# Kernel tuning notes

Hardware: AMD Instinct MI355X
Metric: run time of the kernel (lower is better)

## Reference

```python
import jax, jax.numpy as jnp
import numpy as np

E = 192      # embed_dim
DI = 384     # d_inner = 2*E (mamba default expand=2)
S = 16       # d_state
R = 12       # dt_rank = ceil(E/16)
DEPTH = 4
STRIDE = 4
P = 400      # num_patches = 1600/4
NC = 20
BATCH = 32
EPS = 1e-5


def _rmsnorm(x, w):
    x = x.astype(jnp.float32)
    return x * jax.lax.rsqrt(jnp.mean(x * x, axis=-1, keepdims=True) + EPS) * w


def _mamba_mixer(h, in_w, cw, cb, xpw, dtw, dtb, a_log, d_skip, ow):
    # h: [B, L, E]
    Bsz, Ln, _ = h.shape
    xz = jnp.einsum('ble,de->bld', h, in_w)            # [B,L,2*DI]
    xm, z = xz[..., :DI], xz[..., DI:]
    # causal depthwise conv1d, kernel 4 (left pad 3, truncate to L)
    xp = jnp.pad(xm, ((0, 0), (3, 0), (0, 0)))
    xc = sum(xp[:, k:k + Ln, :] * cw[:, k] for k in range(4)) + cb
    xc = jax.nn.silu(xc)
    xdb = jnp.einsum('bld,rd->blr', xc, xpw)           # [B,L,R+2S]
    dt = jax.nn.softplus(jnp.einsum('blr,dr->bld', xdb[..., :R], dtw) + dtb)
    Bm = xdb[..., R:R + S]
    Cm = xdb[..., R + S:]
    A = -jnp.exp(a_log)                                # [DI,S]

    def step(hst, inp):
        dt_t, b_t, c_t, u_t = inp                      # [B,DI],[B,S],[B,S],[B,DI]
        dA = jnp.exp(dt_t[:, :, None] * A)             # [B,DI,S]
        hst = dA * hst + (dt_t * u_t)[:, :, None] * b_t[:, None, :]
        y_t = jnp.einsum('bdn,bn->bd', hst, c_t)
        return hst, y_t

    h0 = jnp.zeros((Bsz, DI, S), xc.dtype)
    xs = (dt.transpose(1, 0, 2), Bm.transpose(1, 0, 2), Cm.transpose(1, 0, 2), xc.transpose(1, 0, 2))
    _, ys = jax.lax.scan(step, h0, xs)
    y = ys.transpose(1, 0, 2) + xc * d_skip
    y = y * jax.nn.silu(z)
    return jnp.einsum('bld,ed->ble', y, ow)


def _forward(imgs, patch_w, patch_b, cls_token, pos_embed, cnn_w, cnn_b, norm_w,
             in_proj_w, conv_w, conv_b, x_proj_w, dt_proj_w, dt_proj_b, A_log, D,
             out_proj_w, norm_f_w, head_w, head_b):
    Bsz = imgs.shape[0]
    # StrideEmbed: conv1d kernel=stride=4 == reshape + matmul
    x = imgs.reshape(Bsz, P, STRIDE)
    x = jnp.einsum('blk,ek->ble', x, patch_w[:, 0, :]) + patch_b   # [B,P,E]
    x = x + pos_embed[:, :-1, :]
    # depthwise conv1d k=3 pad=1 over length
    xp = jnp.pad(x, ((0, 0), (1, 1), (0, 0)))
    x = sum(xp[:, k:k + P, :] * cnn_w[:, 0, k] for k in range(3)) + cnn_b
    cls = cls_token + pos_embed[:, -1, :]                           # [1,1,E]
    x = jnp.concatenate([x, jnp.broadcast_to(cls, (Bsz, 1, E))], axis=1)  # [B,401,E]

    hidden = x
    residual = None
    for i in range(DEPTH):
        residual = hidden if residual is None else residual + hidden
        hn = _rmsnorm(residual, norm_w[i])
        hidden = _mamba_mixer(hn, in_proj_w[i], conv_w[i], conv_b[i], x_proj_w[i],
                              dt_proj_w[i], dt_proj_b[i], A_log[i], D[i], out_proj_w[i])
    out = _rmsnorm(hidden + residual, norm_f_w)
    v_sem = out[:, -1, :]
    return v_sem @ head_w.T + head_b


def setup_inputs() -> dict:
    key = jax.random.key(0)
    ks = jax.random.split(key, 12)
    n = lambda k, shp, s=0.02: jax.random.normal(k, shp, dtype=jnp.float32) * s
    return {
        'imgs': jax.random.normal(ks[0], (BATCH, 1, 40, 40), jnp.float32),
        'patch_w': n(ks[1], (E, 1, STRIDE), 0.3),
        'patch_b': jnp.zeros((E,), jnp.float32),
        'cls_token': n(ks[2], (1, 1, E)),
        'pos_embed': n(ks[3], (1, P + 1, E)),
        'cnn_w': n(ks[4], (E, 1, 3), 0.3),
        'cnn_b': jnp.zeros((E,), jnp.float32),
        'norm_w': jnp.ones((DEPTH, E), jnp.float32),
        'in_proj_w': n(ks[5], (DEPTH, 2 * DI, E), 0.05),
        'conv_w': n(ks[6], (DEPTH, DI, 4), 0.3),
        'conv_b': jnp.zeros((DEPTH, DI), jnp.float32),
        'x_proj_w': n(ks[7], (DEPTH, R + 2 * S, DI), 0.05),
        'dt_proj_w': n(ks[8], (DEPTH, DI, R), 0.3),
        'dt_proj_b': jnp.log(jnp.expm1(jax.random.uniform(ks[9], (DEPTH, DI), minval=0.001, maxval=0.1))),
        'A_log': jnp.log(jnp.broadcast_to(jnp.arange(1, S + 1, dtype=jnp.float32), (DEPTH, DI, S))),
        'D': jnp.ones((DEPTH, DI), jnp.float32),
        'out_proj_w': n(ks[10], (DEPTH, E, DI), 0.05),
        'norm_f_w': jnp.ones((E,), jnp.float32),
        'head_w': n(ks[11], (NC, E)),
        'head_b': jnp.zeros((NC,), jnp.float32),
    }


def reference(imgs, patch_w, patch_b, cls_token, pos_embed, cnn_w, cnn_b, norm_w,
              in_proj_w, conv_w, conv_b, x_proj_w, dt_proj_w, dt_proj_b, A_log, D,
              out_proj_w, norm_f_w, head_w, head_b):
    return _forward(imgs, patch_w, patch_b, cls_token, pos_embed, cnn_w, cnn_b, norm_w,
                    in_proj_w, conv_w, conv_b, x_proj_w, dt_proj_w, dt_proj_b, A_log, D,
                    out_proj_w, norm_f_w, head_w, head_b)
```

## Files before the change

kernel.cpp:

```cpp
#include <hip/hip_runtime.h>
#include <math.h>

#define E 192
#define DI 384
#define S 16
#define R 12
#define DEPTH 4
#define P 400
#define NC 20
#define BATCH 32
#define L 401
#define NTOK (BATCH * L)
#define CH 32
#define NCH 13

using short8 = __attribute__((ext_vector_type(8))) short;
using float4v = __attribute__((ext_vector_type(4))) float;

__device__ __forceinline__ float siluf(float x) {
    return x / (1.f + __expf(-x));
}
__device__ __forceinline__ float softplusf(float x) {
    return (x > 20.f) ? x : log1pf(__expf(x));
}
__device__ __forceinline__ unsigned short f2bf(float x) {
    unsigned int u = __float_as_uint(x);
    unsigned int r = 0x7fffu + ((u >> 16) & 1u);
    return (unsigned short)((u + r) >> 16);
}
__device__ __forceinline__ float bf2f(unsigned short v) {
    return __uint_as_float(((unsigned int)v) << 16);
}

__global__ void k_embed(const float* __restrict__ imgs, const float* __restrict__ patch_w,
                        const float* __restrict__ patch_b, const float* __restrict__ cls_token,
                        const float* __restrict__ pos_embed, const float* __restrict__ cnn_w,
                        const float* __restrict__ cnn_b, float* __restrict__ resid) {
    int idx = blockIdx.x * blockDim.x + threadIdx.x;
    if (idx >= NTOK * E) return;
    int e = idx % E;
    int bl = idx / E;
    int l = bl % L;
    int b = bl / L;
    float out;
    if (l == P) {
        out = cls_token[e] + pos_embed[(size_t)P * E + e];
    } else {
        float w0 = patch_w[e * 4 + 0], w1 = patch_w[e * 4 + 1];
        float w2 = patch_w[e * 4 + 2], w3 = patch_w[e * 4 + 3];
        float pb = patch_b[e];
        const float* ib = imgs + (size_t)b * 1600;
        auto xe = [&](int ll) -> float {
            const float* ip = ib + ll * 4;
            return ip[0] * w0 + ip[1] * w1 + ip[2] * w2 + ip[3] * w3 + pb +
                   pos_embed[(size_t)ll * E + e];
        };
        float c0 = cnn_w[e * 3 + 0], c1 = cnn_w[e * 3 + 1], c2 = cnn_w[e * 3 + 2];
        float acc = cnn_b[e] + xe(l) * c1;
        if (l > 0) acc += xe(l - 1) * c0;
        if (l < P - 1) acc += xe(l + 1) * c2;
        out = acc;
    }
    resid[idx] = out;
}

__global__ void k_rmsnorm(const float* __restrict__ resid, unsigned short* __restrict__ hn,
                          const float* __restrict__ w) {
    int wave = blockIdx.x * (blockDim.x >> 6) + (threadIdx.x >> 6);
    int lane = threadIdx.x & 63;
    if (wave >= NTOK) return;
    size_t base = (size_t)wave * E;
    float v[3];
    float ss = 0.f;
#pragma unroll
    for (int j = 0; j < 3; j++) {
        int e = lane + j * 64;
        float r = resid[base + e];
        v[j] = r;
        ss += r * r;
    }
#pragma unroll
    for (int off = 32; off > 0; off >>= 1) ss += __shfl_xor(ss, off, 64);
    float scale = rsqrtf(ss * (1.f / (float)E) + 1e-5f);
#pragma unroll
    for (int j = 0; j < 3; j++) {
        int e = lane + j * 64;
        hn[base + e] = f2bf(v[j] * scale * w[e]);
    }
}

__global__ void k_prep(const float* __restrict__ in_proj_w, const float* __restrict__ x_proj_w,
                       const float* __restrict__ out_proj_w, const float* __restrict__ A_log,
                       const float* __restrict__ dt_proj_w,
                       unsigned short* __restrict__ w_in, unsigned short* __restrict__ w_x,
                       unsigned short* __restrict__ w_out, float* __restrict__ negA,
                       float* __restrict__ dtw_t) {
    const int n1 = DEPTH * 2 * DI * E;
    const int n2 = DEPTH * 44 * DI;
    const int n3 = DEPTH * E * DI;
    const int n4 = DEPTH * DI * S;
    const int n5 = DEPTH * DI * R;
    int idx = blockIdx.x * blockDim.x + threadIdx.x;
    if (idx < n1) {
        w_in[idx] = f2bf(in_proj_w[idx]);
    } else if (idx < n1 + n2) {
        int i = idx - n1;
        w_x[i] = f2bf(x_proj_w[i]);
    } else if (idx < n1 + n2 + n3) {
        int i = idx - n1 - n2;
        w_out[i] = f2bf(out_proj_w[i]);
    } else if (idx < n1 + n2 + n3 + n4) {
        int i = idx - n1 - n2 - n3;
        int layer = i / (DI * S);
        int rem = i % (DI * S);
        int n = rem / DI;
        int d = rem % DI;
        negA[i] = -__expf(A_log[(size_t)layer * DI * S + d * S + n]);
    } else if (idx < n1 + n2 + n3 + n4 + n5) {
        int i = idx - n1 - n2 - n3 - n4;
        int layer = i / (DI * R);
        int rem = i % (DI * R);
        int r = rem / DI;
        int d = rem % DI;
        dtw_t[i] = dt_proj_w[(size_t)layer * DI * R + d * R + r];
    }
}

__global__ void k_flag(const float* __restrict__ negA, int* __restrict__ flag) {
    int idx = blockIdx.x * blockDim.x + threadIdx.x;
    if (idx >= DEPTH * DI) return;
    int layer = idx / DI;
    int d = idx % DI;
    const float* base = negA + (size_t)layer * DI * S;
    float a0 = base[d];
    bool ok = true;
#pragma unroll
    for (int n = 1; n < S; n++) {
        float an = base[n * DI + d];
        ok = ok && (fabsf(an - (float)(n + 1) * a0) <= 1e-5f * fabsf(an));
    }
    flag[idx] = ok ? 1 : 0;
}

template <int BM, int BN, int BK, int EPI>
__global__ __launch_bounds__(256) void k_gemm_bf16(const unsigned short* __restrict__ A,
                                                   const unsigned short* __restrict__ W,
                                                   float* __restrict__ C,
                                                   unsigned short* __restrict__ XM,
                                                   unsigned short* __restrict__ Z,
                                                   int M, int N, int K) {
    constexpr int PADK = BK + 8;
    constexpr int MT = BM / 32, NT = BN / 32;
    __shared__ unsigned short As[BM][PADK];
    __shared__ unsigned short Bs[BN][PADK];
    int tid = threadIdx.x;
    int m0 = blockIdx.y * BM, n0 = blockIdx.x * BN;
    int wave = tid >> 6, lane = tid & 63;
    int row16 = lane & 15, quad = lane >> 4;
    int wm0 = (wave >> 1) * (BM / 2), wn0 = (wave & 1) * (BN / 2);

    float4v acc[MT][NT];
#pragma unroll
    for (int i = 0; i < MT; i++)
#pragma unroll
        for (int j = 0; j < NT; j++) acc[i][j] = (float4v){0.f, 0.f, 0.f, 0.f};

    for (int k0 = 0; k0 < K; k0 += BK) {
#pragma unroll
        for (int idx = tid * 8; idx < BM * BK; idx += 256 * 8) {
            int row = idx / BK, col = idx % BK;
            int gm = m0 + row;
            short8 v;
            if (gm < M)
                v = *(const short8*)&A[(size_t)gm * K + k0 + col];
            else
                v = (short8)0;
            *(short8*)&As[row][col] = v;
        }
#pragma unroll
        for (int idx = tid * 8; idx < BN * BK; idx += 256 * 8) {
            int row = idx / BK, col = idx % BK;
            int gn = n0 + row;
            short8 v;
            if (gn < N)
                v = *(const short8*)&W[(size_t)gn * K + k0 + col];
            else
                v = (short8)0;
            *(short8*)&Bs[row][col] = v;
        }
        __syncthreads();
#pragma unroll
        for (int kk = 0; kk < BK; kk += 32) {
            int koff = kk + quad * 8;
            short8 af[MT], bfr[NT];
#pragma unroll
            for (int i = 0; i < MT; i++)
                af[i] = *(const short8*)&As[wm0 + i * 16 + row16][koff];
#pragma unroll
            for (int j = 0; j < NT; j++)
                bfr[j] = *(const short8*)&Bs[wn0 + j * 16 + row16][koff];
#pragma unroll
            for (int i = 0; i < MT; i++)
#pragma unroll
                for (int j = 0; j < NT; j++)
                    acc[i][j] = __builtin_amdgcn_mfma_f32_16x16x32_bf16(af[i], bfr[j],
                                                                        acc[i][j], 0, 0, 0);
        }
        __syncthreads();
    }
#pragma unroll
    for (int i = 0; i < MT; i++) {
#pragma unroll
        for (int j = 0; j < NT; j++) {
#pragma unroll
            for (int r = 0; r < 4; r++) {
                int m = m0 + wm0 + i * 16 + quad * 4 + r;
                int n = n0 + wn0 + j * 16 + row16;
                if (m >= M || n >= N) continue;
                float v = acc[i][j][r];
                if (EPI == 0) {
                    C[(size_t)m * N + n] = v;
                } else if (EPI == 1) {
                    if (n < DI)
                        XM[(size_t)m * DI + n] = f2bf(v);
                    else
                        Z[(size_t)m * DI + (n - DI)] = f2bf(v);
                } else {
                    C[(size_t)m * N + n] += v;
                }
            }
        }
    }
}

__global__ void k_conv(const unsigned short* __restrict__ xm_bf, const float* __restrict__ cw,
                       const float* __restrict__ cb, unsigned short* __restrict__ xc_bf) {
    int idx = blockIdx.x * blockDim.x + threadIdx.x;
    if (idx >= NTOK * DI) return;
    int d = idx % DI;
    int bl = idx / DI;
    int l = bl % L;
    int b = bl / L;
    const unsigned short* base = xm_bf + (size_t)b * L * DI + d;
    float acc = cb[d];
#pragma unroll
    for (int k = 0; k < 4; k++) {
        int ll = l - 3 + k;
        if (ll >= 0) acc += bf2f(base[(size_t)ll * DI]) * cw[d * 4 + k];
    }
    xc_bf[idx] = f2bf(siluf(acc));
}

__global__ __launch_bounds__(384) void k_dtpre(
        const float* __restrict__ xdb, const float* __restrict__ dtw_t,
        const float* __restrict__ dtb, float* __restrict__ dtbuf) {
    int tok = blockIdx.x;
    int d = threadIdx.x;
    const float* xr = xdb + (size_t)tok * 44;
    float acc = dtb[d];
#pragma unroll
    for (int r = 0; r < R; r++) acc += xr[r] * dtw_t[r * DI + d];
    dtbuf[(size_t)tok * DI + d] = softplusf(acc);
}

template <bool LAST>
__global__ __launch_bounds__(384) void k_scanA(
        const unsigned short* __restrict__ xc_bf, const float* __restrict__ xdb,
        const float* __restrict__ dtbuf, const float* __restrict__ negA_l,
        const int* __restrict__ flag_l, const float* __restrict__ Dskip,
        float2* __restrict__ ydt, float* __restrict__ hend) {
    int d = threadIdx.x;
    int ch = blockIdx.x;
    int b = blockIdx.y;
    int t0 = ch * CH;
    int t1 = min(t0 + CH, L);
    bool fast = __all(flag_l[d] != 0);
    float a0 = negA_l[d];
    float a[S];
    if (!fast) {
#pragma unroll
        for (int n = 0; n < S; n++) a[n] = negA_l[n * DI + d];
    }
    float dsk = Dskip[d];
    float h[S] = {};
    float dts = 0.f;
    size_t tok0 = (size_t)b * L + t0;
    float dt_nx = dtbuf[tok0 * DI + d];
    float u_nx = bf2f(xc_bf[tok0 * DI + d]);
    float e1_nx = __expf(a0 * dt_nx);
    for (int t = t0; t < t1; t++) {
        size_t tok = (size_t)b * L + t;
        float dtv = dt_nx, e1v = e1_nx, uu = u_nx;
        if (t + 1 < t1) {
            dt_nx = dtbuf[(tok + 1) * DI + d];
            u_nx = bf2f(xc_bf[(tok + 1) * DI + d]);
            e1_nx = __expf(a0 * dt_nx);
        }
        const float* row = xdb + tok * 44;
        dts += dtv;
        float dtu = dtv * uu;
        float y = uu * dsk;
        if (fast) {
            float p = e1v;
#pragma unroll
            for (int n = 0; n < S; n++) {
                h[n] = p * h[n] + dtu * row[R + n];
                y += h[n] * row[R + S + n];
                p *= e1v;
            }
        } else {
#pragma unroll
            for (int n = 0; n < S; n++) {
                float dA = __expf(dtv * a[n]);
                h[n] = dA * h[n] + dtu * row[R + n];
                y += h[n] * row[R + S + n];
            }
        }
        if (!LAST || t == P || t == t1 - 1) ydt[tok * DI + d] = make_float2(y, dts);
    }
    float* he = hend + ((size_t)(b * NCH + ch) * S) * DI + d;
#pragma unroll
    for (int n = 0; n < S; n++) he[n * DI] = h[n];
}

__global__ __launch_bounds__(384) void k_fixup(
        const unsigned short* __restrict__ z_bf, const float* __restrict__ xdb,
        const float* __restrict__ negA_l, const int* __restrict__ flag_l,
        const float* __restrict__ hend, const float2* __restrict__ ydt,
        unsigned short* __restrict__ y_bf) {
    int d = threadIdx.x;
    int ch = blockIdx.x;
    int b = blockIdx.y;
    bool fast = __all(flag_l[d] != 0);
    float a0 = negA_l[d];
    float a[S];
    if (!fast) {
#pragma unroll
        for (int n = 0; n < S; n++) a[n] = negA_l[n * DI + d];
    }
    float h0[S] = {};
    for (int c = 0; c < ch; c++) {
        size_t o = ((size_t)(b * NCH + c) * S) * DI + d;
        int tlast = min(c * CH + CH, L) - 1;
        float dts = ydt[((size_t)b * L + tlast) * DI + d].y;
        if (fast) {
            float e1c = __expf(a0 * dts);
            float p = e1c;
#pragma unroll
            for (int n = 0; n < S; n++) {
                h0[n] = p * h0[n] + hend[o + n * DI];
                p *= e1c;
            }
        } else {
#pragma unroll
            for (int n = 0; n < S; n++) h0[n] = __expf(dts * a[n]) * h0[n] + hend[o + n * DI];
        }
    }
    int t0 = ch * CH, t1 = min(t0 + CH, L);
    for (int t = t0; t < t1; t++) {
        size_t idx = ((size_t)b * L + t) * DI + d;
        float2 yd = ydt[idx];
        float y = yd.x;
        if (ch != 0) {
            const float* cv = xdb + ((size_t)b * L + t) * 44 + R + S;
            float dts = yd.y;
            float corr = 0.f;
            if (fast) {
                float e1c = __expf(negA_l[d] * dts);
                float p = e1c;
#pragma unroll
                for (int n = 0; n < S; n++) {
                    corr += cv[n] * p * h0[n];
                    p *= e1c;
                }
            } else {
#pragma unroll
                for (int n = 0; n < S; n++)
                    corr += cv[n] * __expf(negA_l[n * DI + d] * dts) * h0[n];
            }
            y += corr;
        }
        float z = bf2f(z_bf[idx]);
        y_bf[idx] = f2bf(y * siluf(z));
    }
}

__global__ __launch_bounds__(384) void k_fixup_last(
        const unsigned short* __restrict__ z_bf, const float* __restrict__ xdb,
        const float* __restrict__ negA_l, const int* __restrict__ flag_l,
        const float* __restrict__ hend, const float2* __restrict__ ydt,
        unsigned short* __restrict__ y32) {
    int b = blockIdx.x;
    int d = threadIdx.x;
    int tok = b * L + P;
    const int ch = P / CH;
    bool fast = __all(flag_l[d] != 0);
    float a0 = negA_l[d];
    float a[S];
    if (!fast) {
#pragma unroll
        for (int n = 0; n < S; n++) a[n] = negA_l[n * DI + d];
    }
    float h0[S] = {};
    for (int c = 0; c < ch; c++) {
        size_t o = ((size_t)(b * NCH + c) * S) * DI + d;
        int tlast = min(c * CH + CH, L) - 1;
        float dts = ydt[((size_t)b * L + tlast) * DI + d].y;
        if (fast) {
            float e1c = __expf(a0 * dts);
            float p = e1c;
#pragma unroll
            for (int n = 0; n < S; n++) {
                h0[n] = p * h0[n] + hend[o + n * DI];
                p *= e1c;
            }
        } else {
#pragma unroll
            for (int n = 0; n < S; n++) h0[n] = __expf(dts * a[n]) * h0[n] + hend[o + n * DI];
        }
    }
    size_t idx = (size_t)tok * DI + d;
    float2 yd = ydt[idx];
    float y = yd.x;
    {
        const float* cv = xdb + (size_t)tok * 44 + R + S;
        float dts = yd.y;
        float corr = 0.f;
        if (fast) {
            float e1c = __expf(negA_l[d] * dts);
            float p = e1c;
#pragma unroll
            for (int n = 0; n < S; n++) {
                corr += cv[n] * p * h0[n];
                p *= e1c;
            }
        } else {
#pragma unroll
            for (int n = 0; n < S; n++)
                corr += cv[n] * __expf(negA_l[n * DI + d] * dts) * h0[n];
        }
        y += corr;
    }
    float z = bf2f(z_bf[idx]);
    y32[(size_t)b * DI + d] = f2bf(y * siluf(z));
}

__global__ void k_head(const float* __restrict__ resid, const float* __restrict__ hidden32,
                       const float* __restrict__ norm_f_w, const float* __restrict__ head_w,
                       const float* __restrict__ head_b, float* __restrict__ out) {
    __shared__ float v[E];
    int b = blockIdx.x;
    int lane = threadIdx.x;
    size_t base = ((size_t)b * L + P) * E;
    float loc[3];
    float ss = 0.f;
#pragma unroll
    for (int j = 0; j < 3; j++) {
        int e = lane + j * 64;
        float x = resid[base + e] + hidden32[(size_t)b * E + e];
        loc[j] = x;
        ss += x * x;
    }
#pragma unroll
    for (int off = 32; off > 0; off >>= 1) ss += __shfl_xor(ss, off, 64);
    float scale = rsqrtf(ss * (1.f / (float)E) + 1e-5f);
#pragma unroll
    for (int j = 0; j < 3; j++) {
        int e = lane + j * 64;
        v[e] = loc[j] * scale * norm_f_w[e];
    }
    __syncthreads();
    if (lane < NC) {
        float acc = head_b[lane];
        for (int e = 0; e < E; e++) acc += v[e] * head_w[lane * E + e];
        out[b * NC + lane] = acc;
    }
}

extern "C" void kernel_launch(void* const* d_in, const int* in_sizes, int n_in,
                              void* d_out, int out_size, void* d_ws, size_t ws_size,
                              hipStream_t stream) {
    const float* imgs      = (const float*)d_in[0];
    const float* patch_w   = (const float*)d_in[1];
    const float* patch_b   = (const float*)d_in[2];
    const float* cls_token = (const float*)d_in[3];
    const float* pos_embed = (const float*)d_in[4];
    const float* cnn_w     = (const float*)d_in[5];
    const float* cnn_b     = (const float*)d_in[6];
    const float* norm_w    = (const float*)d_in[7];
    const float* in_proj_w = (const float*)d_in[8];
    const float* conv_w    = (const float*)d_in[9];
    const float* conv_b    = (const float*)d_in[10];
    const float* x_proj_w  = (const float*)d_in[11];
    const float* dt_proj_w = (const float*)d_in[12];
    const float* dt_proj_b = (const float*)d_in[13];
    const float* A_log     = (const float*)d_in[14];
    const float* Dskip     = (const float*)d_in[15];
    const float* out_proj_w= (const float*)d_in[16];
    const float* norm_f_w  = (const float*)d_in[17];
    const float* head_w    = (const float*)d_in[18];
    const float* head_b    = (const float*)d_in[19];

    float* ws = (float*)d_ws;
    size_t off = 0;
    float* resid  = ws + off; off += (size_t)NTOK * E;
    float* xdb    = ws + off; off += (size_t)NTOK * 44;
    float* dtbuf  = ws + off; off += (size_t)NTOK * DI;
    float* ydt    = ws + off; off += (size_t)NTOK * DI * 2;
    float* hend   = ws + off; off += (size_t)BATCH * NCH * DI * S;
    float* negA   = ws + off; off += (size_t)DEPTH * DI * S;
    float* dtw_t  = ws + off; off += (size_t)DEPTH * DI * R;
    float* hid32  = ws + off; off += (size_t)BATCH * E;
    int*   gflag  = (int*)(ws + off); off += (size_t)DEPTH * DI;
    unsigned short* xm_bf  = (unsigned short*)(ws + off); off += (size_t)NTOK * DI / 2;
    unsigned short* z_bf   = (unsigned short*)(ws + off); off += (size_t)NTOK * DI / 2;
    unsigned short* bf_buf = (unsigned short*)(ws + off); off += (size_t)NTOK * DI / 2;
    unsigned short* y32_bf = (unsigned short*)(ws + off); off += (size_t)BATCH * DI / 2 + 16;
    unsigned short* w_in  = (unsigned short*)(ws + off); off += (size_t)DEPTH * 2 * DI * E / 2;
    unsigned short* w_x   = (unsigned short*)(ws + off); off += (size_t)DEPTH * 44 * DI / 2 + 16;
    unsigned short* w_out = (unsigned short*)(ws + off); off += (size_t)DEPTH * E * DI / 2;

    unsigned short* hn_bf = bf_buf;
    unsigned short* xc_bf = bf_buf;
    unsigned short* y_bf  = bf_buf;

    {
        int ntot = DEPTH * (2 * DI * E + 44 * DI + E * DI + DI * S + DI * R);
        k_prep<<<(ntot + 255) / 256, 256, 0, stream>>>(in_proj_w, x_proj_w, out_proj_w, A_log,
                                                       dt_proj_w, w_in, w_x, w_out, negA,
                                                       dtw_t);
        k_flag<<<(DEPTH * DI + 255) / 256, 256, 0, stream>>>(negA, gflag);
    }

    k_embed<<<(NTOK * E) / 256, 256, 0, stream>>>(imgs, patch_w, patch_b, cls_token,
                                                  pos_embed, cnn_w, cnn_b, resid);

    for (int i = 0; i < DEPTH; i++) {
        k_rmsnorm<<<NTOK / 4, 256, 0, stream>>>(resid, hn_bf, norm_w + i * E);

        {
            dim3 g((2 * DI) / 64, (NTOK + 127) / 128);
            k_gemm_bf16<128, 64, 64, 1><<<g, 256, 0, stream>>>(
                hn_bf, w_in + (size_t)i * 2 * DI * E, nullptr, xm_bf, z_bf, NTOK, 2 * DI, E);
        }
        k_conv<<<(NTOK * DI) / 256, 256, 0, stream>>>(xm_bf, conv_w + (size_t)i * DI * 4,
                                                      conv_b + (size_t)i * DI, xc_bf);
        {
            dim3 g(1, NTOK / 32);
            k_gemm_bf16<32, 64, 128, 0><<<g, 256, 0, stream>>>(
                xc_bf, w_x + (size_t)i * 44 * DI, xdb, nullptr, nullptr, NTOK, 44, DI);
        }
        const float* nA = negA + (size_t)i * DI * S;
        const int* fl = gflag + (size_t)i * DI;
        k_dtpre<<<NTOK, 384, 0, stream>>>(xdb, dtw_t + (size_t)i * DI * R,
                                          dt_proj_b + (size_t)i * DI, dtbuf);
        dim3 g(NCH, BATCH);
        if (i < DEPTH - 1) {
            k_scanA<false><<<g, DI, 0, stream>>>(xc_bf, xdb, dtbuf, nA, fl,
                                                 Dskip + (size_t)i * DI, (float2*)ydt, hend);
            k_fixup<<<g, DI, 0, stream>>>(z_bf, xdb, nA, fl, hend,
                                          (const float2*)ydt, y_bf);
            dim3 go(E / 64, (NTOK + 63) / 64);
            k_gemm_bf16<64, 64, 128, 2><<<go, 256, 0, stream>>>(
                y_bf, w_out + (size_t)i * E * DI, resid, nullptr, nullptr, NTOK, E, DI);
        } else {
            k_scanA<true><<<g, DI, 0, stream>>>(xc_bf, xdb, dtbuf, nA, fl,
                                                Dskip + (size_t)i * DI, (float2*)ydt, hend);
            k_fixup_last<<<BATCH, DI, 0, stream>>>(z_bf, xdb, nA, fl, hend,
                                                   (const float2*)ydt, y32_bf);
            dim3 go(E / 64, 1);
            k_gemm_bf16<32, 64, 128, 0><<<go, 256, 0, stream>>>(
                y32_bf, w_out + (size_t)i * E * DI, hid32, nullptr, nullptr, BATCH, E, DI);
        }
    }

    k_head<<<BATCH, 64, 0, stream>>>(resid, hid32, norm_f_w, head_w, head_b, (float*)d_out);
}
```

Baseline: 746.8 us.

## Fuse chunked scan and fixup into one cooperative kernel with grid sync

Merges the chunked selective-scan and the cross-chunk fixup into a single cooperative kernel. Per-chunk outputs stay in shared memory across two grid-wide syncs instead of going through the global ydt buffer. The prefix combine of chunk end states now runs once per batch in chunk-0 blocks and writes per-chunk initial states, so each chunk no longer redoes the serial combine over all earlier chunks. The change cuts one launch and a large float2 write/read round trip. In exchange it needs 416 co-resident blocks, each holding 48KB of shared memory, and adds grid-sync latency plus a serial 13-step combine phase.

```diff
diff --git a/kernel.cpp b/kernel.cpp
--- a/kernel.cpp
+++ b/kernel.cpp
@@ -1,5 +1,8 @@
 #include <hip/hip_runtime.h>
+#include <hip/hip_cooperative_groups.h>
 #include <math.h>
+
+namespace cg = cooperative_groups;
 
 #define E 192
 #define DI 384
@@ -264,11 +267,14 @@
 }
 
 template <bool LAST>
-__global__ __launch_bounds__(384) void k_scanA(
+__global__ __launch_bounds__(384, 3) void k_scan_fused(
         const unsigned short* __restrict__ xc_bf, const float* __restrict__ xdb,
         const float* __restrict__ dtbuf, const float* __restrict__ negA_l,
         const int* __restrict__ flag_l, const float* __restrict__ Dskip,
-        float2* __restrict__ ydt, float* __restrict__ hend) {
+        const unsigned short* __restrict__ z_bf,
+        float* __restrict__ hend, float* __restrict__ dtlast,
+        float* __restrict__ hinit, unsigned short* __restrict__ y_out) {
+    __shared__ float ysm[CH][DI];
     int d = threadIdx.x;
     int ch = blockIdx.x;
     int b = blockIdx.y;
@@ -282,167 +288,138 @@
         for (int n = 0; n < S; n++) a[n] = negA_l[n * DI + d];
     }
     float dsk = Dskip[d];
-    float h[S] = {};
-    float dts = 0.f;
-    size_t tok0 = (size_t)b * L + t0;
-    float dt_nx = dtbuf[tok0 * DI + d];
-    float u_nx = bf2f(xc_bf[tok0 * DI + d]);
-    float e1_nx = __expf(a0 * dt_nx);
-    for (int t = t0; t < t1; t++) {
-        size_t tok = (size_t)b * L + t;
-        float dtv = dt_nx, e1v = e1_nx, uu = u_nx;
-        if (t + 1 < t1) {
-            dt_nx = dtbuf[(tok + 1) * DI + d];
-            u_nx = bf2f(xc_bf[(tok + 1) * DI + d]);
-            e1_nx = __expf(a0 * dt_nx);
-        }
-        const float* row = xdb + tok * 44;
-        dts += dtv;
-        float dtu = dtv * uu;
-        float y = uu * dsk;
-        if (fast) {
-            float p = e1v;
-#pragma unroll
-            for (int n = 0; n < S; n++) {
-                h[n] = p * h[n] + dtu * row[R + n];
-                y += h[n] * row[R + S + n];
-                p *= e1v;
+
+    {
+        float h[S] = {};
+        float dts = 0.f;
+        size_t tok0 = (size_t)b * L + t0;
+        float dt_nx = dtbuf[tok0 * DI + d];
+        float u_nx = bf2f(xc_bf[tok0 * DI + d]);
+        float e1_nx = __expf(a0 * dt_nx);
+        for (int t = t0; t < t1; t++) {
+            size_t tok = (size_t)b * L + t;
+            float dtv = dt_nx, e1v = e1_nx, uu = u_nx;
+            if (t + 1 < t1) {
+                dt_nx = dtbuf[(tok + 1) * DI + d];
+                u_nx = bf2f(xc_bf[(tok + 1) * DI + d]);
+                e1_nx = __expf(a0 * dt_nx);
             }
-        } else {
-#pragma unroll
-            for (int n = 0; n < S; n++) {
-                float dA = __expf(dtv * a[n]);
-                h[n] = dA * h[n] + dtu * row[R + n];
-                y += h[n] * row[R + S + n];
+            const float* row = xdb + tok * 44;
+            dts += dtv;
+            float dtu = dtv * uu;
+            float y = uu * dsk;
+            if (fast) {
+                float p = e1v;
+#pragma unroll
+                for (int n = 0; n < S; n++) {
+                    h[n] = p * h[n] + dtu * row[R + n];
+                    y += h[n] * row[R + S + n];
+                    p *= e1v;
+                }
+            } else {
+#pragma unroll
+                for (int n = 0; n < S; n++) {
+                    float dA = __expf(dtv * a[n]);
+                    h[n] = dA * h[n] + dtu * row[R + n];
+                    y += h[n] * row[R + S + n];
+                }
             }
-        }
-        if (!LAST || t == P || t == t1 - 1) ydt[tok * DI + d] = make_float2(y, dts);
-    }
-    float* he = hend + ((size_t)(b * NCH + ch) * S) * DI + d;
-#pragma unroll
-    for (int n = 0; n < S; n++) he[n * DI] = h[n];
-}
-
-__global__ __launch_bounds__(384) void k_fixup(
-        const unsigned short* __restrict__ z_bf, const float* __restrict__ xdb,
-        const float* __restrict__ negA_l, const int* __restrict__ flag_l,
-        const float* __restrict__ hend, const float2* __restrict__ ydt,
-        unsigned short* __restrict__ y_bf) {
-    int d = threadIdx.x;
-    int ch = blockIdx.x;
-    int b = blockIdx.y;
-    bool fast = __all(flag_l[d] != 0);
-    float a0 = negA_l[d];
-    float a[S];
-    if (!fast) {
-#pragma unroll
-        for (int n = 0; n < S; n++) a[n] = negA_l[n * DI + d];
-    }
-    float h0[S] = {};
-    for (int c = 0; c < ch; c++) {
-        size_t o = ((size_t)(b * NCH + c) * S) * DI + d;
-        int tlast = min(c * CH + CH, L) - 1;
-        float dts = ydt[((size_t)b * L + tlast) * DI + d].y;
-        if (fast) {
-            float e1c = __expf(a0 * dts);
-            float p = e1c;
-#pragma unroll
-            for (int n = 0; n < S; n++) {
-                h0[n] = p * h0[n] + hend[o + n * DI];
-                p *= e1c;
-            }
-        } else {
-#pragma unroll
-            for (int n = 0; n < S; n++) h0[n] = __expf(dts * a[n]) * h0[n] + hend[o + n * DI];
-        }
-    }
-    int t0 = ch * CH, t1 = min(t0 + CH, L);
-    for (int t = t0; t < t1; t++) {
-        size_t idx = ((size_t)b * L + t) * DI + d;
-        float2 yd = ydt[idx];
-        float y = yd.x;
-        if (ch != 0) {
-            const float* cv = xdb + ((size_t)b * L + t) * 44 + R + S;
-            float dts = yd.y;
-            float corr = 0.f;
+            ysm[t - t0][d] = y;
+        }
+        float* he = hend + ((size_t)(b * NCH + ch) * S) * DI + d;
+#pragma unroll
+        for (int n = 0; n < S; n++) he[n * DI] = h[n];
+        dtlast[(size_t)(b * NCH + ch) * DI + d] = dts;
+    }
+
+    cg::this_grid().sync();
+
+    if (ch == 0) {
+        float hh[S] = {};
+        for (int c = 0; c < NCH; c++) {
+            size_t o = ((size_t)(b * NCH + c) * S) * DI + d;
+#pragma unroll
+            for (int n = 0; n < S; n++) hinit[o + n * DI] = hh[n];
+            float dl = dtlast[(size_t)(b * NCH + c) * DI + d];
             if (fast) {
-                float e1c = __expf(negA_l[d] * dts);
+                float e1c = __expf(a0 * dl);
                 float p = e1c;
 #pragma unroll
                 for (int n = 0; n < S; n++) {
-                    corr += cv[n] * p * h0[n];
+                    hh[n] = p * hh[n] + hend[o + n * DI];
                     p *= e1c;
                 }
             } else {
 #pragma unroll
                 for (int n = 0; n < S; n++)
-                    corr += cv[n] * __expf(negA_l[n * DI + d] * dts) * h0[n];
+                    hh[n] = __expf(dl * a[n]) * hh[n] + hend[o + n * DI];
             }
-            y += corr;
-        }
-        float z = bf2f(z_bf[idx]);
-        y_bf[idx] = f2bf(y * siluf(z));
-    }
-}
-
-__global__ __launch_bounds__(384) void k_fixup_last(
-        const unsigned short* __restrict__ z_bf, const float* __restrict__ xdb,
-        const float* __restrict__ negA_l, const int* __restrict__ flag_l,
-        const float* __restrict__ hend, const float2* __restrict__ ydt,
-        unsigned short* __restrict__ y32) {
-    int b = blockIdx.x;
-    int d = threadIdx.x;
-    int tok = b * L + P;
-    const int ch = P / CH;
-    bool fast = __all(flag_l[d] != 0);
-    float a0 = negA_l[d];
-    float a[S];
-    if (!fast) {
-#pragma unroll
-        for (int n = 0; n < S; n++) a[n] = negA_l[n * DI + d];
-    }
-    float h0[S] = {};
-    for (int c = 0; c < ch; c++) {
-        size_t o = ((size_t)(b * NCH + c) * S) * DI + d;
-        int tlast = min(c * CH + CH, L) - 1;
-        float dts = ydt[((size_t)b * L + tlast) * DI + d].y;
-        if (fast) {
-            float e1c = __expf(a0 * dts);
-            float p = e1c;
-#pragma unroll
-            for (int n = 0; n < S; n++) {
-                h0[n] = p * h0[n] + hend[o + n * DI];
-                p *= e1c;
+        }
+    }
+
+    cg::this_grid().sync();
+
+    float h0[S];
+    if (ch != 0) {
+        size_t o = ((size_t)(b * NCH + ch) * S) * DI + d;
+#pragma unroll
+        for (int n = 0; n < S; n++) h0[n] = hinit[o + n * DI];
+    }
+    if (!LAST) {
+        float ds2 = 0.f;
+        for (int t = t0; t < t1; t++) {
+            size_t idx = ((size_t)b * L + t) * DI + d;
+            ds2 += dtbuf[idx];
+            float y = ysm[t - t0][d];
+            if (ch != 0) {
+                const float* cv = xdb + ((size_t)b * L + t) * 44 + R + S;
+                float corr = 0.f;
+                if (fast) {
+                    float e1c = __expf(a0 * ds2);
+                    float p = e1c;
+#pragma unroll
+                    for (int n = 0; n < S; n++) {
+                        corr += cv[n] * p * h0[n];
+                        p *= e1c;
+                    }
+                } else {
+#pragma unroll
+                    for (int n = 0; n < S; n++)
+                        corr += cv[n] * __expf(negA_l[n * DI + d] * ds2) * h0[n];
+                }
+                y += corr;
             }
-        } else {
-#pragma unroll
-            for (int n = 0; n < S; n++) h0[n] = __expf(dts * a[n]) * h0[n] + hend[o + n * DI];
-        }
-    }
-    size_t idx = (size_t)tok * DI + d;
-    float2 yd = ydt[idx];
-    float y = yd.x;
-    {
-        const float* cv = xdb + (size_t)tok * 44 + R + S;
-        float dts = yd.y;
-        float corr = 0.f;
-        if (fast) {
-            float e1c = __expf(negA_l[d] * dts);
-            float p = e1c;
-#pragma unroll
-            for (int n = 0; n < S; n++) {
-                corr += cv[n] * p * h0[n];
-                p *= e1c;
+            float z = bf2f(z_bf[idx]);
+            y_out[idx] = f2bf(y * siluf(z));
+        }
+    } else {
+        if (ch == P / CH) {
+            float ds2 = 0.f;
+            for (int t = t0; t <= P; t++) ds2 += dtbuf[((size_t)b * L + t) * DI + d];
+            size_t idx = ((size_t)b * L + P) * DI + d;
+            float y = ysm[P - t0][d];
+            {
+                const float* cv = xdb + ((size_t)b * L + P) * 44 + R + S;
+                float corr = 0.f;
+                if (fast) {
+                    float e1c = __expf(a0 * ds2);
+                    float p = e1c;
+#pragma unroll
+                    for (int n = 0; n < S; n++) {
+                        corr += cv[n] * p * h0[n];
+                        p *= e1c;
+                    }
+                } else {
+#pragma unroll
+                    for (int n = 0; n < S; n++)
+                        corr += cv[n] * __expf(negA_l[n * DI + d] * ds2) * h0[n];
+                }
+                y += corr;
             }
-        } else {
-#pragma unroll
-            for (int n = 0; n < S; n++)
-                corr += cv[n] * __expf(negA_l[n * DI + d] * dts) * h0[n];
-        }
-        y += corr;
-    }
-    float z = bf2f(z_bf[idx]);
-    y32[(size_t)b * DI + d] = f2bf(y * siluf(z));
+            float z = bf2f(z_bf[idx]);
+            y_out[(size_t)b * DI + d] = f2bf(y * siluf(z));
+        }
+    }
 }
 
 __global__ void k_head(const float* __restrict__ resid, const float* __restrict__ hidden32,
@@ -506,8 +483,9 @@
     float* resid  = ws + off; off += (size_t)NTOK * E;
     float* xdb    = ws + off; off += (size_t)NTOK * 44;
     float* dtbuf  = ws + off; off += (size_t)NTOK * DI;
-    float* ydt    = ws + off; off += (size_t)NTOK * DI * 2;
     float* hend   = ws + off; off += (size_t)BATCH * NCH * DI * S;
+    float* hinit  = ws + off; off += (size_t)BATCH * NCH * DI * S;
+    float* dtlast = ws + off; off += (size_t)BATCH * NCH * DI;
     float* negA   = ws + off; off += (size_t)DEPTH * DI * S;
     float* dtw_t  = ws + off; off += (size_t)DEPTH * DI * R;
     float* hid32  = ws + off; off += (size_t)BATCH * E;
@@ -554,20 +532,35 @@
         const int* fl = gflag + (size_t)i * DI;
         k_dtpre<<<NTOK, 384, 0, stream>>>(xdb, dtw_t + (size_t)i * DI * R,
                                           dt_proj_b + (size_t)i * DI, dtbuf);
-        dim3 g(NCH, BATCH);
+
+        {
+            const unsigned short* p_xc = xc_bf;
+            const float* p_xdb = xdb;
+            const float* p_dt = dtbuf;
+            const float* p_nA = nA;
+            const int* p_fl = fl;
+            const float* p_dsk = Dskip + (size_t)i * DI;
+            const unsigned short* p_z = z_bf;
+            float* p_hend = hend;
+            float* p_dtl = dtlast;
+            float* p_hinit = hinit;
+            unsigned short* p_y = (i < DEPTH - 1) ? y_bf : y32_bf;
+            void* kargs[] = {(void*)&p_xc, (void*)&p_xdb, (void*)&p_dt, (void*)&p_nA,
+                             (void*)&p_fl, (void*)&p_dsk, (void*)&p_z, (void*)&p_hend,
+                             (void*)&p_dtl, (void*)&p_hinit, (void*)&p_y};
+            if (i < DEPTH - 1)
+                hipLaunchCooperativeKernel((const void*)k_scan_fused<false>,
+                                           dim3(NCH, BATCH), dim3(DI), kargs, 0, stream);
+            else
+                hipLaunchCooperativeKernel((const void*)k_scan_fused<true>,
+                                           dim3(NCH, BATCH), dim3(DI), kargs, 0, stream);
+        }
+
         if (i < DEPTH - 1) {
-            k_scanA<false><<<g, DI, 0, stream>>>(xc_bf, xdb, dtbuf, nA, fl,
-                                                 Dskip + (size_t)i * DI, (float2*)ydt, hend);
-            k_fixup<<<g, DI, 0, stream>>>(z_bf, xdb, nA, fl, hend,
-                                          (const float2*)ydt, y_bf);
             dim3 go(E / 64, (NTOK + 63) / 64);
             k_gemm_bf16<64, 64, 128, 2><<<go, 256, 0, stream>>>(
                 y_bf, w_out + (size_t)i * E * DI, resid, nullptr, nullptr, NTOK, E, DI);
         } else {
-            k_scanA<true><<<g, DI, 0, stream>>>(xc_bf, xdb, dtbuf, nA, fl,
-                                                Dskip + (size_t)i * DI, (float2*)ydt, hend);
-            k_fixup_last<<<BATCH, DI, 0, stream>>>(z_bf, xdb, nA, fl, hend,
-                                                   (const float2*)ydt, y32_bf);
             dim3 go(E / 64, 1);
             k_gemm_bf16<32, 64, 128, 0><<<go, 256, 0, stream>>>(
                 y32_bf, w_out + (size_t)i * E * DI, hid32, nullptr, nullptr, BATCH, E, DI);
```

Result: slower. 1.239 ms (+66.0%).
